# Optimization experiments

Hardware: AMD Instinct MI355X
Metric: run time of the kernel (lower is better)

## Reference

```python
import jax, jax.numpy as jnp
import numpy as np

B, T = 32, 64
INPUT_DIM, EMB, HA, HB, NUM_CLASS = 4894, 128, 128, 128, 1
D_IN = EMB + 1  # use_time=True appends scalar time feature


def gru_cell(x, h, Wih, Whh, bih, bhh):
    # torch nn.GRU cell semantics, gate order (r, z, n)
    gi = x @ Wih.T + bih
    gh = h @ Whh.T + bhh
    ir, iz, i_n = jnp.split(gi, 3, axis=-1)
    hr, hz, hn = jnp.split(gh, 3, axis=-1)
    r = jax.nn.sigmoid(ir + hr)
    z = jax.nn.sigmoid(iz + hz)
    n = jnp.tanh(i_n + r * hn)
    return (1.0 - z) * n + z * h


def setup_inputs():
    key = jax.random.key(0)
    ks = jax.random.split(key, 14)
    f32 = jnp.float32
    s = lambda k, sh, sc: (jax.random.normal(k, sh) * sc).astype(f32)
    return {
        "x": jax.random.uniform(ks[0], (B, T, INPUT_DIM), dtype=f32),
        "t": jax.random.uniform(ks[1], (B, T), dtype=f32),
        "lengths": jax.random.randint(ks[2], (B,), 1, T + 1),
        "W_emb": s(ks[3], (EMB, INPUT_DIM), 0.02),
        "Wih_a": s(ks[4], (3 * HA, D_IN), 0.05),
        "Whh_a": s(ks[5], (3 * HA, HA), 0.05),
        "bih_a": jnp.zeros((3 * HA,), f32),
        "bhh_a": jnp.zeros((3 * HA,), f32),
        "Wih_b": s(ks[6], (3 * HB, D_IN), 0.05),
        "Whh_b": s(ks[7], (3 * HB, HB), 0.05),
        "bih_b": jnp.zeros((3 * HB,), f32),
        "bhh_b": jnp.zeros((3 * HB,), f32),
        "w_alpha": s(ks[8], (1, HA), 0.1),
        "b_alpha": jnp.zeros((1,), f32),
        "W_beta": s(ks[9], (EMB, HB), 0.1),
        "b_beta": jnp.zeros((EMB,), f32),
        "W_out": s(ks[10], (NUM_CLASS, EMB), 0.1),
        "b_out": jnp.zeros((NUM_CLASS,), f32),
    }


def reference(x, t, lengths, W_emb, Wih_a, Whh_a, bih_a, bhh_a,
              Wih_b, Whh_b, bih_b, bhh_b, w_alpha, b_alpha,
              W_beta, b_beta, W_out, b_out):
    # embedding (dropout is identity in inference)
    emb = x @ W_emb.T                                   # [B,T,E]
    temb = jnp.concatenate([emb, t[..., None]], axis=-1)  # [B,T,E+1]

    # reversed-prefix tensor: R[b,i,k] = temb[b, i-k] for k<=i else 0
    i_idx = jnp.arange(T)[:, None]
    k_idx = jnp.arange(T)[None, :]
    src = i_idx - k_idx                                  # [T,T]
    valid = (src >= 0)
    src_c = jnp.clip(src, 0)
    vmask = valid[None, :, :, None].astype(emb.dtype)
    R = jnp.take(temb, src_c, axis=1) * vmask            # [B,T,T,D_IN]
    E_rev = jnp.take(emb, src_c, axis=1) * vmask         # [B,T,T,E]

    # run alpha/beta GRUs along the prefix axis k (causal, so zero padding
    # at k>i never affects the k<=i outputs that we keep)
    R_k = jnp.moveaxis(R, 2, 0)                          # [Tk,B,T,D_IN]
    h0a = jnp.zeros((B, T, HA), emb.dtype)
    h0b = jnp.zeros((B, T, HB), emb.dtype)

    def step(carry, xk):
        ha, hb = carry
        ha = gru_cell(xk, ha, Wih_a, Whh_a, bih_a, bhh_a)
        hb = gru_cell(xk, hb, Wih_b, Whh_b, bih_b, bhh_b)
        return (ha, hb), (ha, hb)

    _, (Ha, Hb) = jax.lax.scan(step, (h0a, h0b), R_k)
    Ha = jnp.moveaxis(Ha, 0, 2)                          # [B,T,Tk,HA]
    Hb = jnp.moveaxis(Hb, 0, 2)                          # [B,T,Tk,HB]

    # attention over the i+1 prefix positions
    scores = (Ha @ w_alpha.T + b_alpha)[..., 0]          # [B,T,Tk]
    scores = jnp.where(valid[None], scores, jnp.float32(-1e9))
    alpha = jax.nn.softmax(scores, axis=-1)
    beta = jnp.tanh(Hb @ W_beta.T + b_beta)              # [B,T,Tk,E]

    c = jnp.einsum('btk,btke,btke->bte', alpha, beta, E_rev)
    row_valid = (jnp.arange(T)[None, :] < lengths[:, None]).astype(c.dtype)
    c = c * row_valid[..., None]                         # zero where i >= lengths[b]

    logits = c @ W_out.T + b_out                         # [B,T,1]
    return logits[..., 0]
```

## Files before the change

### kernel.cpp

```cpp
#include <hip/hip_runtime.h>
#include <hip/hip_bf16.h>

#define DEVI __device__ __forceinline__

typedef __attribute__((ext_vector_type(8))) short short8;
typedef __attribute__((ext_vector_type(8))) unsigned short ushort8;
typedef __attribute__((ext_vector_type(4))) unsigned short ushort4v;
typedef __attribute__((ext_vector_type(4))) float f32x4;

static constexpr int TT = 64, KIN = 4894, KINP = 4896, E = 128;
static constexpr float L2E = 1.4426950408889634f;

DEVI unsigned short f2bf(float f) {
    union { float f; unsigned u; } v; v.f = f;
    unsigned r = v.u + 0x7fffu + ((v.u >> 16) & 1u);
    return (unsigned short)(r >> 16);
}
DEVI float sigm2(float x) { return __builtin_amdgcn_rcpf(1.f + __builtin_amdgcn_exp2f(-x)); }
DEVI float tanh2(float x) { return 1.f - 2.f * __builtin_amdgcn_rcpf(__builtin_amdgcn_exp2f(x + x) + 1.f); }

__global__ void prep_kernel(const float* __restrict__ Wemb,
                            const float* __restrict__ Wih_a, const float* __restrict__ Wih_b,
                            const float* __restrict__ Whh_a, const float* __restrict__ Whh_b,
                            const float* __restrict__ Wbeta,
                            unsigned short* __restrict__ wembbf, unsigned short* __restrict__ wihbf,
                            unsigned short* __restrict__ whhbf, unsigned short* __restrict__ wbetabf) {
    int job = blockIdx.x * blockDim.x + threadIdx.x;
    const int JWE = 128 * 612, JWIH = 768 * 16, JWHH = 768 * 16, JWB = 128 * 16;
    if (job < JWE) {
        int row = job / 612, c8 = (job % 612) * 8;
        ushort8 v;
        #pragma unroll
        for (int jj = 0; jj < 8; ++jj) { int c = c8 + jj; v[jj] = (c < KIN) ? f2bf(Wemb[(long)row * KIN + c]) : (unsigned short)0; }
        *(ushort8*)(wembbf + (long)row * KINP + c8) = v;
        return;
    }
    job -= JWE;
    if (job < JWIH) {
        int g = job / 16, c8 = (job % 16) * 8;
        const float* src = (g < 384) ? (Wih_a + (long)g * 129) : (Wih_b + (long)(g - 384) * 129);
        ushort8 v;
        #pragma unroll
        for (int jj = 0; jj < 8; ++jj) v[jj] = f2bf(src[c8 + jj] * L2E);
        *(ushort8*)(wihbf + (long)g * 128 + c8) = v;
        return;
    }
    job -= JWIH;
    if (job < JWHH) {
        int g = job / 16, c8 = (job % 16) * 8;
        const float* src = (g < 384) ? (Whh_a + (long)g * 128) : (Whh_b + (long)(g - 384) * 128);
        ushort8 v;
        #pragma unroll
        for (int jj = 0; jj < 8; ++jj) v[jj] = f2bf(src[c8 + jj] * L2E);
        *(ushort8*)(whhbf + (long)g * 128 + c8) = v;
        return;
    }
    job -= JWHH;
    if (job < JWB) {
        int e = job / 16, c8 = (job % 16) * 8;
        ushort8 v;
        #pragma unroll
        for (int jj = 0; jj < 8; ++jj) v[jj] = f2bf(Wbeta[(long)e * 128 + c8 + jj] * L2E);
        *(ushort8*)(wbetabf + (long)e * 128 + c8) = v;
    }
}

__global__ __launch_bounds__(256) void emb_gemm(const float* __restrict__ x,
                                                const unsigned short* __restrict__ wembbf,
                                                float* __restrict__ pout) {
    const int ks = blockIdx.x & 3, m0 = (blockIdx.x >> 2) * 16;
    const int w = threadIdx.x >> 6, l = threadIdx.x & 63, lr = l & 15, lo = l >> 4;
    const int n0 = (2 * w) * 16 + lr, n1 = (2 * w + 1) * 16 + lr;
    const float* xrow = x + (long)(m0 + lr) * KIN;
    const int k0 = ks * 1216;
    const int nfull = 38;
    f32x4 acc0 = {0, 0, 0, 0}, acc1 = {0, 0, 0, 0};
    #pragma unroll 2
    for (int kt = 0; kt < nfull; ++kt) {
        int k = k0 + kt * 32 + lo * 8;
        float2 x0 = *(const float2*)(xrow + k);
        float2 x1 = *(const float2*)(xrow + k + 2);
        float2 x2 = *(const float2*)(xrow + k + 4);
        float2 x3 = *(const float2*)(xrow + k + 6);
        short8 a;
        a[0] = (short)f2bf(x0.x); a[1] = (short)f2bf(x0.y);
        a[2] = (short)f2bf(x1.x); a[3] = (short)f2bf(x1.y);
        a[4] = (short)f2bf(x2.x); a[5] = (short)f2bf(x2.y);
        a[6] = (short)f2bf(x3.x); a[7] = (short)f2bf(x3.y);
        short8 b0 = *(const short8*)(wembbf + (long)n0 * KINP + k);
        short8 b1 = *(const short8*)(wembbf + (long)n1 * KINP + k);
        acc0 = __builtin_amdgcn_mfma_f32_16x16x32_bf16(a, b0, acc0, 0, 0, 0);
        acc1 = __builtin_amdgcn_mfma_f32_16x16x32_bf16(a, b1, acc1, 0, 0, 0);
    }
    if (ks == 3) {
        int k = 4864 + lo * 8;
        short8 a;
        #pragma unroll
        for (int jj = 0; jj < 8; ++jj) { int c = k + jj; a[jj] = (c < KIN) ? (short)f2bf(xrow[c]) : (short)0; }
        short8 b0 = *(const short8*)(wembbf + (long)n0 * KINP + k);
        short8 b1 = *(const short8*)(wembbf + (long)n1 * KINP + k);
        acc0 = __builtin_amdgcn_mfma_f32_16x16x32_bf16(a, b0, acc0, 0, 0, 0);
        acc1 = __builtin_amdgcn_mfma_f32_16x16x32_bf16(a, b1, acc1, 0, 0, 0);
    }
    float* pbase = pout + (long)ks * 2048 * E;
    #pragma unroll
    for (int r = 0; r < 4; ++r) {
        int m = m0 + lo * 4 + r;
        pbase[(long)m * E + n0] = acc0[r];
        pbase[(long)m * E + n1] = acc1[r];
    }
}

__global__ __launch_bounds__(256) void emb_reduce(const float* __restrict__ pout,
                                                  float* __restrict__ emb, unsigned short* __restrict__ embbf) {
    const long idx = (long)blockIdx.x * 256 + threadIdx.x;
    const long base = idx * 4;
    f32x4 s = *(const f32x4*)(pout + base);
    #pragma unroll
    for (int ks = 1; ks < 4; ++ks) {
        f32x4 v = *(const f32x4*)(pout + (long)ks * 2048 * E + base);
        s[0] += v[0]; s[1] += v[1]; s[2] += v[2]; s[3] += v[3];
    }
    *(f32x4*)(emb + base) = s;
    ushort4v h;
    #pragma unroll
    for (int jj = 0; jj < 4; ++jj) h[jj] = f2bf(s[jj]);
    *(ushort4v*)(embbf + base) = h;
}

__global__ __launch_bounds__(256) void gi_gemm(const unsigned short* __restrict__ embbf,
                                               const unsigned short* __restrict__ wihbf,
                                               const float* __restrict__ Wih_a, const float* __restrict__ Wih_b,
                                               const float* __restrict__ t,
                                               const float* __restrict__ bih_a, const float* __restrict__ bih_b,
                                               const float* __restrict__ bhh_a, const float* __restrict__ bhh_b,
                                               float* __restrict__ Gi3) {
    const int m0 = blockIdx.x * 16;
    const int w = threadIdx.x >> 6, l = threadIdx.x & 63, lr = l & 15, lo = l >> 4;
    f32x4 acc[12];
    #pragma unroll
    for (int nl = 0; nl < 12; ++nl) acc[nl] = (f32x4){0, 0, 0, 0};
    #pragma unroll
    for (int kt = 0; kt < 4; ++kt) {
        int k = kt * 32 + lo * 8;
        short8 a0 = *(const short8*)(embbf + (long)(m0 + lr) * E + k);
        #pragma unroll
        for (int nl = 0; nl < 12; ++nl) {
            int n = (w * 12 + nl) * 16 + lr;
            short8 bf = *(const short8*)(wihbf + (long)n * 128 + k);
            acc[nl] = __builtin_amdgcn_mfma_f32_16x16x32_bf16(a0, bf, acc[nl], 0, 0, 0);
        }
    }
    #pragma unroll
    for (int nl = 0; nl < 12; ++nl) {
        int n = (w * 12 + nl) * 16 + lr;
        int gru = (n >= 384) ? 1 : 0;
        int nn = n - gru * 384;
        int gt = nn >> 7, u = nn & 127;
        float bias = (gru ? bih_b[nn] : bih_a[nn]);
        if (gt < 2) bias += (gru ? bhh_b[nn] : bhh_a[nn]);
        float cw = (n < 384) ? Wih_a[(long)n * 129 + 128] : Wih_b[(long)(n - 384) * 129 + 128];
        #pragma unroll
        for (int r = 0; r < 4; ++r) {
            int tok = m0 + lo * 4 + r;
            Gi3[((long)(tok * 2 + gru) * 128 + u) * 4 + gt] = acc[nl][r] + (bias + t[tok] * cw) * L2E;
        }
    }
}

__global__ __launch_bounds__(512) __attribute__((amdgpu_waves_per_eu(2, 2)))
void retain_rec(const unsigned short* __restrict__ whhbf, const unsigned short* __restrict__ wbetabf,
                const float* __restrict__ Gi3, const float* __restrict__ emb,
                const float* __restrict__ bhh_a, const float* __restrict__ bhh_b,
                const float* __restrict__ w_alpha, const float* __restrict__ b_alpha,
                const float* __restrict__ b_beta, const float* __restrict__ Wout,
                float* __restrict__ p_g, float* __restrict__ d_g) {
    const int tid = threadIdx.x;
    const int w = tid >> 6, l = tid & 63, lr = l & 15, lo = l >> 4;
    const int i = blockIdx.x >> 2, q = (blockIdx.x >> 1) & 1, g = blockIdx.x & 1;
    const int u = w * 16 + lr;

    __shared__ __align__(16) unsigned short Hbf[2][16][128];
    __shared__ float red[2][8][16];

    for (int idx = tid; idx < 2 * 16 * 128; idx += 512) (&Hbf[0][0][0])[idx] = 0;

    short8 Wf[3][4];
    #pragma unroll
    for (int gt = 0; gt < 3; ++gt)
        #pragma unroll
        for (int kt = 0; kt < 4; ++kt)
            Wf[gt][kt] = *(const short8*)(whhbf + (long)(g * 384 + gt * 128 + u) * 128 + kt * 32 + lo * 8);

    short8 Xf[4];
    float bbetL = 0.f, wo = 0.f;
    if (g) {
        #pragma unroll
        for (int kt = 0; kt < 4; ++kt)
            Xf[kt] = *(const short8*)(wbetabf + (long)u * 128 + kt * 32 + lo * 8);
        bbetL = b_beta[u] * L2E;
        wo = Wout[u];
    } else {
        #pragma unroll
        for (int kt = 0; kt < 4; ++kt) {
            short8 z;
            #pragma unroll
            for (int jj = 0; jj < 8; ++jj) z[jj] = 0;
            Xf[kt] = z;
        }
    }

    const float bhnL = (g ? bhh_b : bhh_a)[256 + u] * L2E;
    const float waL = g ? 0.f : w_alpha[u] * L2E;
    const float balL = b_alpha[0] * L2E;

    float h_old[4] = {0, 0, 0, 0};
    __syncthreads();

    for (int n = 0; n <= i + 2; ++n) {
        const int rb = n & 1, wb = rb ^ 1;
        const bool do_gate = (n <= i);
        const bool do_post = (n >= 1) && (n <= i + 1);

        if (w == 0 && l < 16) {
            const long row = (long)(q * 16 + l) * 64 + i;
            if (!g) {
                if (do_post) {
                    float s = balL;
                    #pragma unroll
                    for (int ww = 0; ww < 8; ++ww) s += red[wb][ww][l];
                    p_g[row * 64 + (n - 1)] = __builtin_amdgcn_exp2f(s);
                }
            } else {
                if (n >= 2) {
                    float d = 0.f;
                    #pragma unroll
                    for (int ww = 0; ww < 8; ++ww) d += red[wb][ww][l];
                    d_g[row * 64 + (n - 2)] = d;
                }
            }
        }

        f32x4 giv[4];
        if (do_gate) {
            const int j = i - n;
            #pragma unroll
            for (int r = 0; r < 4; ++r) {
                int tok = (q * 16 + lo * 4 + r) * 64 + j;
                giv[r] = *(const f32x4*)(Gi3 + ((long)(tok * 2 + g) * 128 + u) * 4);
            }
        }
        float ev[4];
        if (g && do_post) {
            const int j2 = i - n + 1;
            #pragma unroll
            for (int r = 0; r < 4; ++r) {
                int tok = (q * 16 + lo * 4 + r) * 64 + j2;
                ev[r] = emb[(long)tok * E + u];
            }
        }

        short8 Af[4];
        if (do_gate || (g && do_post)) {
            #pragma unroll
            for (int kt = 0; kt < 4; ++kt) {
                int sw = (kt * 32 + lo * 8) ^ ((lr & 7) * 8);
                Af[kt] = *(const short8*)(&Hbf[rb][lr][sw]);
            }
        }

        f32x4 gh0 = {0, 0, 0, 0}, gh1 = {0, 0, 0, 0}, gh2 = {bhnL, bhnL, bhnL, bhnL};
        f32x4 xacc = {0, 0, 0, 0};
        if (do_gate) {
            #pragma unroll
            for (int kt = 0; kt < 4; ++kt) {
                gh0 = __builtin_amdgcn_mfma_f32_16x16x32_bf16(Af[kt], Wf[0][kt], gh0, 0, 0, 0);
                gh1 = __builtin_amdgcn_mfma_f32_16x16x32_bf16(Af[kt], Wf[1][kt], gh1, 0, 0, 0);
                gh2 = __builtin_amdgcn_mfma_f32_16x16x32_bf16(Af[kt], Wf[2][kt], gh2, 0, 0, 0);
            }
        }
        if (g && do_post) {
            #pragma unroll
            for (int kt = 0; kt < 4; ++kt)
                xacc = __builtin_amdgcn_mfma_f32_16x16x32_bf16(Af[kt], Xf[kt], xacc, 0, 0, 0);
            float dp[4];
            #pragma unroll
            for (int r = 0; r < 4; ++r) dp[r] = tanh2(xacc[r] + bbetL) * ev[r] * wo;
            #pragma unroll
            for (int r = 0; r < 4; ++r) {
                dp[r] += __shfl_xor(dp[r], 1);
                dp[r] += __shfl_xor(dp[r], 2);
                dp[r] += __shfl_xor(dp[r], 4);
                dp[r] += __shfl_xor(dp[r], 8);
            }
            if (lr == 0) {
                #pragma unroll
                for (int r = 0; r < 4; ++r) red[rb][w][lo * 4 + r] = dp[r];
            }
        }

        if (do_gate) {
            float sp[4];
            #pragma unroll
            for (int r = 0; r < 4; ++r) {
                f32x4 gv = giv[r];
                float rr = sigm2(gv[0] + gh0[r]);
                float zz = sigm2(gv[1] + gh1[r]);
                float nn = tanh2(gv[2] + rr * gh2[r]);
                float h = nn + zz * (h_old[r] - nn);
                h_old[r] = h;
                int c = lo * 4 + r;
                Hbf[wb][c][u ^ ((c & 7) * 8)] = f2bf(h);
                sp[r] = h * waL;
            }
            if (!g) {
                #pragma unroll
                for (int r = 0; r < 4; ++r) {
                    sp[r] += __shfl_xor(sp[r], 1);
                    sp[r] += __shfl_xor(sp[r], 2);
                    sp[r] += __shfl_xor(sp[r], 4);
                    sp[r] += __shfl_xor(sp[r], 8);
                }
                if (lr == 0) {
                    #pragma unroll
                    for (int r = 0; r < 4; ++r) red[rb][w][lo * 4 + r] = sp[r];
                }
            }
        }

        __syncthreads();
    }
}

__global__ __launch_bounds__(512) void reduce_out(const float* __restrict__ p_g, const float* __restrict__ d_g,
                                                  const int* __restrict__ lengths, const float* __restrict__ b_out,
                                                  float* __restrict__ out) {
    const int w = threadIdx.x >> 6, l = threadIdx.x & 63;
    const int row = blockIdx.x * 8 + w;
    const int b = row >> 6, i = row & 63;
    float p = (l <= i) ? p_g[(long)row * 64 + l] : 0.f;
    float d = (l <= i) ? d_g[(long)row * 64 + l] : 0.f;
    float pd = p * d;
    #pragma unroll
    for (int off = 1; off < 64; off <<= 1) {
        p += __shfl_xor(p, off);
        pd += __shfl_xor(pd, off);
    }
    if (l == 0) {
        float val = (i < lengths[b]) ? pd / p + b_out[0] : b_out[0];
        out[row] = val;
    }
}

extern "C" void kernel_launch(void* const* d_in, const int* in_sizes, int n_in,
                              void* d_out, int out_size, void* d_ws, size_t ws_size,
                              hipStream_t stream) {
    (void)in_sizes; (void)n_in; (void)out_size; (void)ws_size;
    const float* x       = (const float*)d_in[0];
    const float* t       = (const float*)d_in[1];
    const int*   len     = (const int*)d_in[2];
    const float* Wemb    = (const float*)d_in[3];
    const float* Wih_a   = (const float*)d_in[4];
    const float* Whh_a   = (const float*)d_in[5];
    const float* bih_a   = (const float*)d_in[6];
    const float* bhh_a   = (const float*)d_in[7];
    const float* Wih_b   = (const float*)d_in[8];
    const float* Whh_b   = (const float*)d_in[9];
    const float* bih_b   = (const float*)d_in[10];
    const float* bhh_b   = (const float*)d_in[11];
    const float* w_alpha = (const float*)d_in[12];
    const float* b_alpha = (const float*)d_in[13];
    const float* W_beta  = (const float*)d_in[14];
    const float* b_beta  = (const float*)d_in[15];
    const float* W_out   = (const float*)d_in[16];
    const float* b_out   = (const float*)d_in[17];

    char* ws = (char*)d_ws;
    float*          emb     = (float*)(ws + 0);
    unsigned short* embbf   = (unsigned short*)(ws + 1048576);
    float*          Gi3     = (float*)(ws + 1572864);
    unsigned short* wembbf  = (unsigned short*)(ws + 9961472);
    unsigned short* wihbf   = (unsigned short*)(ws + 11214848);
    unsigned short* whhbf   = (unsigned short*)(ws + 11411456);
    unsigned short* wbetabf = (unsigned short*)(ws + 11608064);
    float*          p_g     = (float*)(ws + 11640832);
    float*          d_g     = (float*)(ws + 12165120);
    float*          pout    = (float*)(ws + 12689408);

    const int jobs = 128 * 612 + 768 * 16 + 768 * 16 + 128 * 16;
    prep_kernel<<<(jobs + 255) / 256, 256, 0, stream>>>(Wemb, Wih_a, Wih_b, Whh_a, Whh_b, W_beta,
                                                        wembbf, wihbf, whhbf, wbetabf);
    emb_gemm<<<512, 256, 0, stream>>>(x, wembbf, pout);
    emb_reduce<<<256, 256, 0, stream>>>(pout, emb, embbf);
    gi_gemm<<<128, 256, 0, stream>>>(embbf, wihbf, Wih_a, Wih_b, t, bih_a, bih_b, bhh_a, bhh_b, Gi3);
    retain_rec<<<256, 512, 0, stream>>>(whhbf, wbetabf, Gi3, emb, bhh_a, bhh_b,
                                        w_alpha, b_alpha, b_beta, W_out, p_g, d_g);
    reduce_out<<<256, 512, 0, stream>>>(p_g, d_g, len, b_out, (float*)d_out);
}
```

Before: 165.4 us.

## Prefetch next-step Gi3/emb loads and stage per-step outputs in LDS

```diff
diff --git a/kernel.cpp b/kernel.cpp
--- a/kernel.cpp
+++ b/kernel.cpp
@@ -182,6 +182,7 @@
 
     __shared__ __align__(16) unsigned short Hbf[2][16][128];
     __shared__ float red[2][8][16];
+    __shared__ float pd_s[16][66];
 
     for (int idx = tid; idx < 2 * 16 * 128; idx += 512) (&Hbf[0][0][0])[idx] = 0;
 
@@ -215,48 +216,66 @@
     const float balL = b_alpha[0] * L2E;
 
     float h_old[4] = {0, 0, 0, 0};
+
+    f32x4 giv[4];
+    #pragma unroll
+    for (int r = 0; r < 4; ++r) {
+        int tok = (q * 16 + lo * 4 + r) * 64 + i;
+        giv[r] = *(const f32x4*)(Gi3 + ((long)(tok * 2 + g) * 128 + u) * 4);
+    }
+    float ev[4] = {0, 0, 0, 0};
+    if (g) {
+        #pragma unroll
+        for (int r = 0; r < 4; ++r) {
+            int tok = (q * 16 + lo * 4 + r) * 64 + i;
+            ev[r] = emb[(long)tok * E + u];
+        }
+    }
+
     __syncthreads();
 
-    for (int n = 0; n <= i + 2; ++n) {
+    const int iend = i + 1 + g;
+    for (int n = 0; n <= iend; ++n) {
         const int rb = n & 1, wb = rb ^ 1;
         const bool do_gate = (n <= i);
         const bool do_post = (n >= 1) && (n <= i + 1);
 
+        f32x4 givn[4];
+        float evn[4];
+        const bool ld_gi = (n < i);
+        const bool ld_ev = g && (n <= i);
+        if (ld_gi) {
+            const int jn = i - n - 1;
+            #pragma unroll
+            for (int r = 0; r < 4; ++r) {
+                int tok = (q * 16 + lo * 4 + r) * 64 + jn;
+                givn[r] = *(const f32x4*)(Gi3 + ((long)(tok * 2 + g) * 128 + u) * 4);
+            }
+        }
+        if (ld_ev) {
+            const int j2n = i - n;
+            #pragma unroll
+            for (int r = 0; r < 4; ++r) {
+                int tok = (q * 16 + lo * 4 + r) * 64 + j2n;
+                evn[r] = emb[(long)tok * E + u];
+            }
+        }
+
         if (w == 0 && l < 16) {
-            const long row = (long)(q * 16 + l) * 64 + i;
             if (!g) {
                 if (do_post) {
                     float s = balL;
                     #pragma unroll
                     for (int ww = 0; ww < 8; ++ww) s += red[wb][ww][l];
-                    p_g[row * 64 + (n - 1)] = __builtin_amdgcn_exp2f(s);
+                    pd_s[l][n - 1] = __builtin_amdgcn_exp2f(s);
                 }
             } else {
                 if (n >= 2) {
                     float d = 0.f;
                     #pragma unroll
                     for (int ww = 0; ww < 8; ++ww) d += red[wb][ww][l];
-                    d_g[row * 64 + (n - 2)] = d;
+                    pd_s[l][n - 2] = d;
                 }
-            }
-        }
-
-        f32x4 giv[4];
-        if (do_gate) {
-            const int j = i - n;
-            #pragma unroll
-            for (int r = 0; r < 4; ++r) {
-                int tok = (q * 16 + lo * 4 + r) * 64 + j;
-                giv[r] = *(const f32x4*)(Gi3 + ((long)(tok * 2 + g) * 128 + u) * 4);
-            }
-        }
-        float ev[4];
-        if (g && do_post) {
-            const int j2 = i - n + 1;
-            #pragma unroll
-            for (int r = 0; r < 4; ++r) {
-                int tok = (q * 16 + lo * 4 + r) * 64 + j2;
-                ev[r] = emb[(long)tok * E + u];
             }
         }
 
@@ -328,7 +347,25 @@
             }
         }
 
+        if (ld_gi) {
+            #pragma unroll
+            for (int r = 0; r < 4; ++r) giv[r] = givn[r];
+        }
+        if (ld_ev) {
+            #pragma unroll
+            for (int r = 0; r < 4; ++r) ev[r] = evn[r];
+        }
+
         __syncthreads();
+    }
+
+    float* dst = g ? d_g : p_g;
+    for (int idx = tid; idx < 16 * 64; idx += 512) {
+        int c = idx >> 6, kk = idx & 63;
+        if (kk <= i) {
+            long row = (long)(q * 16 + c) * 64 + i;
+            dst[row * 64 + kk] = pd_s[c][kk];
+        }
     }
 }
 
```

Result: faster. 160.3 us (-3.1%).

## Transpose recurrence MFMA layout, reduce via MFMA, prefetch inputs, lighter barrier

Applied to the files above, without the earlier changes.

```diff
diff --git a/kernel.cpp b/kernel.cpp
--- a/kernel.cpp
+++ b/kernel.cpp
@@ -6,6 +6,7 @@
 typedef __attribute__((ext_vector_type(8))) short short8;
 typedef __attribute__((ext_vector_type(8))) unsigned short ushort8;
 typedef __attribute__((ext_vector_type(4))) unsigned short ushort4v;
+typedef __attribute__((ext_vector_type(2))) unsigned int u32x2;
 typedef __attribute__((ext_vector_type(4))) float f32x4;
 
 static constexpr int TT = 64, KIN = 4894, KINP = 4896, E = 128;
@@ -18,6 +19,22 @@
 }
 DEVI float sigm2(float x) { return __builtin_amdgcn_rcpf(1.f + __builtin_amdgcn_exp2f(-x)); }
 DEVI float tanh2(float x) { return 1.f - 2.f * __builtin_amdgcn_rcpf(__builtin_amdgcn_exp2f(x + x) + 1.f); }
+
+DEVI void bar_lds() {
+    asm volatile("s_waitcnt lgkmcnt(0)" ::: "memory");
+    __builtin_amdgcn_s_barrier();
+}
+
+DEVI short8 cvt8(const float* __restrict__ p, float s) {
+    float2 v0 = *(const float2*)p, v1 = *(const float2*)(p + 2);
+    float2 v2 = *(const float2*)(p + 4), v3 = *(const float2*)(p + 6);
+    short8 r;
+    r[0] = (short)f2bf(v0.x * s); r[1] = (short)f2bf(v0.y * s);
+    r[2] = (short)f2bf(v1.x * s); r[3] = (short)f2bf(v1.y * s);
+    r[4] = (short)f2bf(v2.x * s); r[5] = (short)f2bf(v2.y * s);
+    r[6] = (short)f2bf(v3.x * s); r[7] = (short)f2bf(v3.y * s);
+    return r;
+}
 
 __global__ void prep_kernel(const float* __restrict__ Wemb,
                             const float* __restrict__ Wih_a, const float* __restrict__ Wih_b,
@@ -73,20 +90,11 @@
     const int n0 = (2 * w) * 16 + lr, n1 = (2 * w + 1) * 16 + lr;
     const float* xrow = x + (long)(m0 + lr) * KIN;
     const int k0 = ks * 1216;
-    const int nfull = 38;
     f32x4 acc0 = {0, 0, 0, 0}, acc1 = {0, 0, 0, 0};
     #pragma unroll 2
-    for (int kt = 0; kt < nfull; ++kt) {
+    for (int kt = 0; kt < 38; ++kt) {
         int k = k0 + kt * 32 + lo * 8;
-        float2 x0 = *(const float2*)(xrow + k);
-        float2 x1 = *(const float2*)(xrow + k + 2);
-        float2 x2 = *(const float2*)(xrow + k + 4);
-        float2 x3 = *(const float2*)(xrow + k + 6);
-        short8 a;
-        a[0] = (short)f2bf(x0.x); a[1] = (short)f2bf(x0.y);
-        a[2] = (short)f2bf(x1.x); a[3] = (short)f2bf(x1.y);
-        a[4] = (short)f2bf(x2.x); a[5] = (short)f2bf(x2.y);
-        a[6] = (short)f2bf(x3.x); a[7] = (short)f2bf(x3.y);
+        short8 a = cvt8(xrow + k, 1.f);
         short8 b0 = *(const short8*)(wembbf + (long)n0 * KINP + k);
         short8 b1 = *(const short8*)(wembbf + (long)n1 * KINP + k);
         acc0 = __builtin_amdgcn_mfma_f32_16x16x32_bf16(a, b0, acc0, 0, 0, 0);
@@ -178,10 +186,11 @@
     const int tid = threadIdx.x;
     const int w = tid >> 6, l = tid & 63, lr = l & 15, lo = l >> 4;
     const int i = blockIdx.x >> 2, q = (blockIdx.x >> 1) & 1, g = blockIdx.x & 1;
-    const int u = w * 16 + lr;
+    const int u0 = w * 16 + lo * 4;
 
     __shared__ __align__(16) unsigned short Hbf[2][16][128];
-    __shared__ float red[2][8][16];
+    __shared__ __align__(16) unsigned short Mld[2][16][128];
+    __shared__ float pd_s[16][66];
 
     for (int idx = tid; idx < 2 * 16 * 128; idx += 512) (&Hbf[0][0][0])[idx] = 0;
 
@@ -190,78 +199,70 @@
     for (int gt = 0; gt < 3; ++gt)
         #pragma unroll
         for (int kt = 0; kt < 4; ++kt)
-            Wf[gt][kt] = *(const short8*)(whhbf + (long)(g * 384 + gt * 128 + u) * 128 + kt * 32 + lo * 8);
-
+            Wf[gt][kt] = *(const short8*)(whhbf + (long)(g * 384 + gt * 128 + w * 16 + lr) * 128 + kt * 32 + lo * 8);
     short8 Xf[4];
-    float bbetL = 0.f, wo = 0.f;
+    #pragma unroll
+    for (int kt = 0; kt < 4; ++kt)
+        Xf[kt] = g ? *(const short8*)(wbetabf + (long)(w * 16 + lr) * 128 + kt * 32 + lo * 8)
+                   : cvt8(w_alpha + kt * 32 + lo * 8, L2E);
+    short8 ones;
+    #pragma unroll
+    for (int jj = 0; jj < 8; ++jj) ones[jj] = (short)0x3F80;
+
+    const float* bhhG = g ? bhh_b : bhh_a;
+    f32x4 bhn4 = *(const f32x4*)(bhhG + 256 + u0);
+    #pragma unroll
+    for (int r = 0; r < 4; ++r) bhn4[r] *= L2E;
+    f32x4 bb4 = {0, 0, 0, 0}, wo4 = {0, 0, 0, 0};
     if (g) {
-        #pragma unroll
-        for (int kt = 0; kt < 4; ++kt)
-            Xf[kt] = *(const short8*)(wbetabf + (long)u * 128 + kt * 32 + lo * 8);
-        bbetL = b_beta[u] * L2E;
-        wo = Wout[u];
-    } else {
-        #pragma unroll
-        for (int kt = 0; kt < 4; ++kt) {
-            short8 z;
-            #pragma unroll
-            for (int jj = 0; jj < 8; ++jj) z[jj] = 0;
-            Xf[kt] = z;
-        }
-    }
-
-    const float bhnL = (g ? bhh_b : bhh_a)[256 + u] * L2E;
-    const float waL = g ? 0.f : w_alpha[u] * L2E;
+        bb4 = *(const f32x4*)(b_beta + u0);
+        #pragma unroll
+        for (int r = 0; r < 4; ++r) bb4[r] *= L2E;
+        wo4 = *(const f32x4*)(Wout + u0);
+    }
     const float balL = b_alpha[0] * L2E;
 
     float h_old[4] = {0, 0, 0, 0};
+
+    const int tok0 = (q * 16 + lr) * 64 + i;
+    const f32x4* gp = (const f32x4*)Gi3 + ((long)(tok0 * 2 + g) * 128 + u0);
+    const float* ep = emb + (long)tok0 * E + u0;
+    f32x4 giv[4];
+    #pragma unroll
+    for (int r = 0; r < 4; ++r) giv[r] = gp[r];
+    f32x4 ev = {0, 0, 0, 0};
+
     __syncthreads();
 
-    for (int n = 0; n <= i + 2; ++n) {
+    const int iend = i + 1 + g;
+    for (int n = 0; n <= iend; ++n) {
         const int rb = n & 1, wb = rb ^ 1;
         const bool do_gate = (n <= i);
         const bool do_post = (n >= 1) && (n <= i + 1);
-
-        if (w == 0 && l < 16) {
-            const long row = (long)(q * 16 + l) * 64 + i;
-            if (!g) {
-                if (do_post) {
-                    float s = balL;
-                    #pragma unroll
-                    for (int ww = 0; ww < 8; ++ww) s += red[wb][ww][l];
-                    p_g[row * 64 + (n - 1)] = __builtin_amdgcn_exp2f(s);
-                }
-            } else {
-                if (n >= 2) {
-                    float d = 0.f;
-                    #pragma unroll
-                    for (int ww = 0; ww < 8; ++ww) d += red[wb][ww][l];
-                    d_g[row * 64 + (n - 2)] = d;
-                }
+        const bool ld_gi = (n < i);
+        const bool ld_ev = g && (n <= i);
+
+        f32x4 givn[4], evn;
+        if (ld_gi) {
+            gp -= 256;
+            #pragma unroll
+            for (int r = 0; r < 4; ++r) givn[r] = gp[r];
+        }
+        if (ld_ev) { evn = *(const f32x4*)ep; ep -= E; }
+
+        if (g && w == 0 && n >= 2) {
+            f32x4 dacc = {0, 0, 0, 0};
+            #pragma unroll
+            for (int kt = 0; kt < 4; ++kt) {
+                int sw = (kt * 32 + lo * 8) ^ ((lr & 7) * 8);
+                short8 bm = *(const short8*)(&Mld[wb][lr][sw]);
+                dacc = __builtin_amdgcn_mfma_f32_16x16x32_bf16(ones, bm, dacc, 0, 0, 0);
             }
-        }
-
-        f32x4 giv[4];
-        if (do_gate) {
-            const int j = i - n;
-            #pragma unroll
-            for (int r = 0; r < 4; ++r) {
-                int tok = (q * 16 + lo * 4 + r) * 64 + j;
-                giv[r] = *(const f32x4*)(Gi3 + ((long)(tok * 2 + g) * 128 + u) * 4);
-            }
-        }
-        float ev[4];
-        if (g && do_post) {
-            const int j2 = i - n + 1;
-            #pragma unroll
-            for (int r = 0; r < 4; ++r) {
-                int tok = (q * 16 + lo * 4 + r) * 64 + j2;
-                ev[r] = emb[(long)tok * E + u];
-            }
+            if (lo == 0) pd_s[lr][n - 2] = dacc[0];
         }
 
         short8 Af[4];
-        if (do_gate || (g && do_post)) {
+        if (do_gate || do_post) {
             #pragma unroll
             for (int kt = 0; kt < 4; ++kt) {
                 int sw = (kt * 32 + lo * 8) ^ ((lr & 7) * 8);
@@ -269,66 +270,69 @@
             }
         }
 
-        f32x4 gh0 = {0, 0, 0, 0}, gh1 = {0, 0, 0, 0}, gh2 = {bhnL, bhnL, bhnL, bhnL};
-        f32x4 xacc = {0, 0, 0, 0};
+        f32x4 gh0 = {0, 0, 0, 0}, gh1 = {0, 0, 0, 0}, gh2 = bhn4;
         if (do_gate) {
             #pragma unroll
             for (int kt = 0; kt < 4; ++kt) {
-                gh0 = __builtin_amdgcn_mfma_f32_16x16x32_bf16(Af[kt], Wf[0][kt], gh0, 0, 0, 0);
-                gh1 = __builtin_amdgcn_mfma_f32_16x16x32_bf16(Af[kt], Wf[1][kt], gh1, 0, 0, 0);
-                gh2 = __builtin_amdgcn_mfma_f32_16x16x32_bf16(Af[kt], Wf[2][kt], gh2, 0, 0, 0);
+                gh0 = __builtin_amdgcn_mfma_f32_16x16x32_bf16(Wf[0][kt], Af[kt], gh0, 0, 0, 0);
+                gh1 = __builtin_amdgcn_mfma_f32_16x16x32_bf16(Wf[1][kt], Af[kt], gh1, 0, 0, 0);
+                gh2 = __builtin_amdgcn_mfma_f32_16x16x32_bf16(Wf[2][kt], Af[kt], gh2, 0, 0, 0);
             }
         }
-        if (g && do_post) {
+
+        if (do_post) {
+            f32x4 xacc = {0, 0, 0, 0};
             #pragma unroll
             for (int kt = 0; kt < 4; ++kt)
-                xacc = __builtin_amdgcn_mfma_f32_16x16x32_bf16(Af[kt], Xf[kt], xacc, 0, 0, 0);
-            float dp[4];
-            #pragma unroll
-            for (int r = 0; r < 4; ++r) dp[r] = tanh2(xacc[r] + bbetL) * ev[r] * wo;
-            #pragma unroll
-            for (int r = 0; r < 4; ++r) {
-                dp[r] += __shfl_xor(dp[r], 1);
-                dp[r] += __shfl_xor(dp[r], 2);
-                dp[r] += __shfl_xor(dp[r], 4);
-                dp[r] += __shfl_xor(dp[r], 8);
+                xacc = __builtin_amdgcn_mfma_f32_16x16x32_bf16(Xf[kt], Af[kt], xacc, 0, 0, 0);
+            if (!g) {
+                if (w == 0 && lo == 0) pd_s[lr][n - 1] = __builtin_amdgcn_exp2f(xacc[0] + balL);
+            } else {
+                float m0v = tanh2(xacc[0] + bb4[0]) * ev[0] * wo4[0];
+                float m1v = tanh2(xacc[1] + bb4[1]) * ev[1] * wo4[1];
+                float m2v = tanh2(xacc[2] + bb4[2]) * ev[2] * wo4[2];
+                float m3v = tanh2(xacc[3] + bb4[3]) * ev[3] * wo4[3];
+                unsigned mp0, mp1;
+                asm("v_cvt_pk_bf16_f32 %0, %1, %2" : "=v"(mp0) : "v"(m0v), "v"(m1v));
+                asm("v_cvt_pk_bf16_f32 %0, %1, %2" : "=v"(mp1) : "v"(m2v), "v"(m3v));
+                *(u32x2*)(&Mld[rb][lr][u0 ^ ((lr & 7) * 8)]) = (u32x2){mp0, mp1};
             }
-            if (lr == 0) {
-                #pragma unroll
-                for (int r = 0; r < 4; ++r) red[rb][w][lo * 4 + r] = dp[r];
-            }
         }
 
         if (do_gate) {
-            float sp[4];
+            float hn[4];
             #pragma unroll
             for (int r = 0; r < 4; ++r) {
                 f32x4 gv = giv[r];
                 float rr = sigm2(gv[0] + gh0[r]);
                 float zz = sigm2(gv[1] + gh1[r]);
-                float nn = tanh2(gv[2] + rr * gh2[r]);
-                float h = nn + zz * (h_old[r] - nn);
+                float nv = tanh2(gv[2] + rr * gh2[r]);
+                float h = nv + zz * (h_old[r] - nv);
                 h_old[r] = h;
-                int c = lo * 4 + r;
-                Hbf[wb][c][u ^ ((c & 7) * 8)] = f2bf(h);
-                sp[r] = h * waL;
+                hn[r] = h;
             }
-            if (!g) {
-                #pragma unroll
-                for (int r = 0; r < 4; ++r) {
-                    sp[r] += __shfl_xor(sp[r], 1);
-                    sp[r] += __shfl_xor(sp[r], 2);
-                    sp[r] += __shfl_xor(sp[r], 4);
-                    sp[r] += __shfl_xor(sp[r], 8);
-                }
-                if (lr == 0) {
-                    #pragma unroll
-                    for (int r = 0; r < 4; ++r) red[rb][w][lo * 4 + r] = sp[r];
-                }
-            }
-        }
-
-        __syncthreads();
+            unsigned p0, p1;
+            asm("v_cvt_pk_bf16_f32 %0, %1, %2" : "=v"(p0) : "v"(hn[0]), "v"(hn[1]));
+            asm("v_cvt_pk_bf16_f32 %0, %1, %2" : "=v"(p1) : "v"(hn[2]), "v"(hn[3]));
+            *(u32x2*)(&Hbf[wb][lr][u0 ^ ((lr & 7) * 8)]) = (u32x2){p0, p1};
+        }
+
+        if (ld_gi) {
+            #pragma unroll
+            for (int r = 0; r < 4; ++r) giv[r] = givn[r];
+        }
+        if (ld_ev) ev = evn;
+
+        bar_lds();
+    }
+
+    float* dst = g ? d_g : p_g;
+    for (int idx = tid; idx < 16 * 64; idx += 512) {
+        int c = idx >> 6, kk = idx & 63;
+        if (kk <= i) {
+            long row = (long)(q * 16 + c) * 64 + i;
+            dst[row * 64 + kk] = pd_s[c][kk];
+        }
     }
 }
 
```

After: 164.5 us. About the same (-0.5%).
